# Optimization experiments

Measured on AMD Instinct MI355X. Metric: run time of the kernel, lower is better.

## Reference

```python
import jax, jax.numpy as jnp
import numpy as np

B, S, D, H = 16, 512, 1024, 4096
TOP_K = H // 4  # default: hidden_dim // 4


def setup_inputs() -> dict:
    key = jax.random.key(0)
    ks = jax.random.split(key, 11)
    s = lambda fan_in: 1.0 / np.sqrt(fan_in)
    return {
        "inputs": jax.random.normal(ks[0], (B, S, D), jnp.float32),
        "up_w": jax.random.uniform(ks[1], (H, D), jnp.float32, -s(D), s(D)),
        "up_b": jax.random.uniform(ks[2], (H,), jnp.float32, -s(D), s(D)),
        "gate_w1": jax.random.uniform(ks[3], (H, D), jnp.float32, -s(D), s(D)),
        "gate_b1": jax.random.uniform(ks[4], (H,), jnp.float32, -s(D), s(D)),
        "gate_w2": jax.random.uniform(ks[5], (H, H), jnp.float32, -s(H), s(H)),
        "gate_b2": jax.random.uniform(ks[6], (H,), jnp.float32, -s(H), s(H)),
        "mod_w": jax.random.uniform(ks[7], (H, D), jnp.float32, -s(D), s(D)),
        "mod_b": jax.random.uniform(ks[8], (H,), jnp.float32, -s(D), s(D)),
        "down_w": jax.random.uniform(ks[9], (D, H), jnp.float32, -s(H), s(H)),
        "down_b": jax.random.uniform(ks[10], (D,), jnp.float32, -s(H), s(H)),
    }


def reference(inputs, up_w, up_b, gate_w1, gate_b1, gate_w2, gate_b2,
              mod_w, mod_b, down_w, down_b):
    b, s_len, d = inputs.shape
    h_dim = up_w.shape[0]
    # gate MLP -> scores [B, S, H]
    scores = jax.nn.relu(jnp.einsum('bsd,hd->bsh', inputs, gate_w1) + gate_b1)
    scores = jnp.einsum('bsh,gh->bsg', scores, gate_w2) + gate_b2
    flat = scores.reshape(b, s_len * h_dim)
    k = min(TOP_K * s_len, s_len * h_dim)
    _, flat_idx = jax.lax.top_k(flat, k)                    # [B, k]
    hidden_idx = flat_idx % h_dim                           # [B, k]
    # mask[b, h] = True if row h of up.weight was overwritten by mod.weight
    # (duplicate indices write the same value, so set-semantics are exact)
    mask = jnp.zeros((b, h_dim), bool).at[
        jnp.arange(b)[:, None], hidden_idx].set(True)       # [B, H]
    # Instead of materializing per-batch [B,H,D] weights, compute both shared-
    # weight GEMMs and select per (batch, hidden) row — identical math.
    h_up = jnp.einsum('bsd,hd->bsh', inputs, up_w) + up_b
    h_mod = jnp.einsum('bsd,hd->bsh', inputs, mod_w) + mod_b
    h = jnp.where(mask[:, None, :], h_mod, h_up)            # [B, S, H]
    h = jax.nn.silu(h)
    # dropout is identity in eval/reference mode
    return jnp.einsum('bsh,dh->bsd', h, down_w) + down_b
```

## Files before the change

kernel.cpp:

```cpp
#include <hip/hip_runtime.h>
#include <cstdint>

typedef __attribute__((ext_vector_type(4))) _Float16 f16x4;
typedef __attribute__((ext_vector_type(8))) _Float16 f16x8;
typedef __attribute__((ext_vector_type(4))) float f32x4;

#define D_DIM 1024
#define H_DIM 4096
#define BS_ROWS 8192
#define K_SEL 524288u
#define CAND_CAP 32768u

__device__ __forceinline__ unsigned lkey(float v){
  float u = fmaf(v, 67108864.f, 268435456.f);
  u = fminf(fmaxf(u, 0.f), 536870911.f);
  return (unsigned)u;
}

__device__ __forceinline__ void gload16(const _Float16* g, _Float16* l){
  __builtin_amdgcn_global_load_lds(
      (const __attribute__((address_space(1))) void*)g,
      (__attribute__((address_space(3))) void*)l, 16, 0, 0);
}

template<int N> __device__ __forceinline__ void waitcnt_vm(){
  if      constexpr (N == 0) asm volatile("s_waitcnt vmcnt(0)" ::: "memory");
  else if constexpr (N == 4) asm volatile("s_waitcnt vmcnt(4)" ::: "memory");
  else if constexpr (N == 6) asm volatile("s_waitcnt vmcnt(6)" ::: "memory");
  else                       asm volatile("s_waitcnt vmcnt(8)" ::: "memory");
}

__device__ __forceinline__ size_t img_g32(int row, int k8, int nkt32){
  int p = (row & 127) >> 1;
  int s = (((row & 1) << 2) | (k8 & 3)) ^ (p & 7);
  return ((size_t)((row >> 7) * nkt32 + (k8 >> 2)) << 9) + (p << 3) + s;
}

__global__ __launch_bounds__(256)
void pack_all(const float* __restrict__ X, const float* __restrict__ g1w,
              const float* __restrict__ g2w, const float* __restrict__ upw,
              const float* __restrict__ modw, const float* __restrict__ dww,
              _Float16* __restrict__ Xhi, _Float16* __restrict__ Xlo,
              _Float16* __restrict__ G1hi, _Float16* __restrict__ G1lo,
              _Float16* __restrict__ G2hi, _Float16* __restrict__ G2lo,
              _Float16* __restrict__ UPhi, _Float16* __restrict__ MODhi,
              _Float16* __restrict__ DWhi)
{
  unsigned g = blockIdx.x * 256u + threadIdx.x;
  const float* W; _Float16* hi; _Float16* lo = nullptr;
  int k8s, n32; unsigned base;
  if      (g < 1048576u){ W=X;    hi=Xhi;  lo=Xlo;  k8s=7; n32=32;  base=0u;        }
  else if (g < 1572864u){ W=g1w;  hi=G1hi; lo=G1lo; k8s=7; n32=32;  base=1048576u; }
  else if (g < 3670016u){ W=g2w;  hi=G2hi; lo=G2lo; k8s=9; n32=128; base=1572864u; }
  else if (g < 4194304u){ W=upw;  hi=UPhi;          k8s=7; n32=32;  base=3670016u; }
  else if (g < 4718592u){ W=modw; hi=MODhi;         k8s=7; n32=32;  base=4194304u; }
  else                  { W=dww;  hi=DWhi;          k8s=9; n32=128; base=4718592u; }
  g -= base;
  int row = (int)(g >> k8s), k8 = (int)(g & ((1u << k8s) - 1u));
  const float* src = W + ((size_t)row << (k8s + 3)) + (k8 << 3);
  float4 f0 = *(const float4*)src, f1 = *(const float4*)(src + 4);
  float ff[8] = {f0.x,f0.y,f0.z,f0.w,f1.x,f1.y,f1.z,f1.w};
  f16x8 hv, lv;
  #pragma unroll
  for (int i = 0; i < 8; i++){
    hv[i] = (_Float16)ff[i];
    lv[i] = (_Float16)(ff[i] - (float)hv[i]);
  }
  size_t d = img_g32(row, k8, n32) << 3;
  *(f16x8*)&hi[d] = hv;
  if (lo) *(f16x8*)&lo[d] = lv;
}

enum { MODE_G1 = 0, MODE_G2 = 1, MODE_UPMOD = 2, MODE_DOWN = 3 };

template<int MODE>
__global__ __launch_bounds__(256)
void gemm_t(const _Float16* __restrict__ Ahi, const _Float16* __restrict__ Alo,
            const _Float16* __restrict__ Bhi, const _Float16* __restrict__ Blo,
            const float* __restrict__ bias0, const float* __restrict__ bias1,
            const unsigned* __restrict__ mask,
            _Float16* __restrict__ Chi, _Float16* __restrict__ Clo,
            float* __restrict__ C32,
            unsigned* __restrict__ keys, unsigned* __restrict__ Mkey,
            unsigned* __restrict__ hist,
            int N, int K, int m_img_base, int c_row_base, int batch_base)
{
  constexpr int NSEG = (MODE == MODE_G1) ? 3 : 1;
  constexpr bool BSEL = (MODE == MODE_UPMOD);
  constexpr int NLD = (NSEG == 3) ? 8 : (BSEL ? 6 : 4);
  __shared__ __align__(16) _Float16 sA [2][4096];
  __shared__ __align__(16) _Float16 sB [2][4096];
  __shared__ __align__(16) _Float16 sAl[NSEG >= 2 ? 2 : 1][NSEG >= 2 ? 4096 : 8];
  __shared__ __align__(16) _Float16 sBl[(NSEG == 3 || BSEL) ? 2 : 1][(NSEG == 3 || BSEL) ? 4096 : 8];
  __shared__ unsigned lh[MODE == MODE_G2 ? 4096 : 1];

  const int nbx = gridDim.x;
  int wg = blockIdx.y * nbx + blockIdx.x;
  const int nwg = nbx * gridDim.y;
  wg = (wg & 7) * (nwg >> 3) + (wg >> 3);
  const int bx = wg % nbx, by = wg / nbx;

  const int tid = threadIdx.x;
  const int lane = tid & 63;
  const int w  = tid >> 6;
  const int wr = w >> 1, wc = w & 1;
  const int lr = lane & 15;
  const int q  = lane >> 4;

  const int m0 = m_img_base + by * 128;
  const int n0 = bx * 128;
  const int nkt = K >> 5;
  const size_t arow = (size_t)(m0 >> 7) * nkt;
  const size_t brow = (size_t)(n0 >> 7) * nkt;

  const _Float16* bbase[4];
  if (BSEL){
    const int bb = m0 >> 9;
    #pragma unroll
    for (int i = 0; i < 4; i++){
      int row = wc*64 + i*16 + lr;
      bbase[i] = mask[bb * H_DIM + n0 + row] ? &sBl[0][0] : &sB[0][0];
    }
    waitcnt_vm<0>();
  }

  f32x4 acc[4][4];
  #pragma unroll
  for (int i = 0; i < 4; i++)
    #pragma unroll
    for (int j = 0; j < 4; j++) acc[i][j] = (f32x4){0.f,0.f,0.f,0.f};

  const int soff = (((((lr & 1) << 2) | q) ^ (lr >> 1)) << 3);

  auto STAGE = [&](int buf, int kt){
    const _Float16* at = Ahi + ((arow + kt) << 12);
    #pragma unroll
    for (int j = 0; j < 2; j++)
      gload16(at + ((w*2 + j) << 9) + (lane << 3), &sA[buf][(w*2 + j) << 9]);
    if (NSEG >= 2){
      const _Float16* alt = Alo + ((arow + kt) << 12);
      const _Float16* bht = Bhi + ((brow + kt) << 12);
      #pragma unroll
      for (int j = 0; j < 2; j++){
        gload16(alt + ((w*2 + j) << 9) + (lane << 3), &sAl[buf][(w*2 + j) << 9]);
        gload16(bht + ((w*2 + j) << 9) + (lane << 3), &sB [buf][(w*2 + j) << 9]);
      }
      if (NSEG == 3){
        const _Float16* blt = Blo + ((brow + kt) << 12);
        #pragma unroll
        for (int j = 0; j < 2; j++)
          gload16(blt + ((w*2 + j) << 9) + (lane << 3), &sBl[buf][(w*2 + j) << 9]);
      }
    } else if (BSEL){
      const _Float16* bht = Bhi + ((brow + kt) << 12);
      const _Float16* blt = Blo + ((brow + kt) << 12);
      #pragma unroll
      for (int j = 0; j < 2; j++){
        gload16(bht + ((w*2 + j) << 9) + (lane << 3), &sB [buf][(w*2 + j) << 9]);
        gload16(blt + ((w*2 + j) << 9) + (lane << 3), &sBl[buf][(w*2 + j) << 9]);
      }
    } else {
      const _Float16* bht = Bhi + ((brow + kt) << 12);
      #pragma unroll
      for (int j = 0; j < 2; j++)
        gload16(bht + ((w*2 + j) << 9) + (lane << 3), &sB[buf][(w*2 + j) << 9]);
    }
  };

  STAGE(0, 0);
  int cur = 0;
  for (int kt = 0; kt < nkt; ++kt){
    if (kt + 1 < nkt){ STAGE(cur ^ 1, kt + 1); waitcnt_vm<NLD>(); }
    else             { waitcnt_vm<0>(); }
    __builtin_amdgcn_s_barrier();
    __builtin_amdgcn_sched_barrier(0);

    f16x8 fah[4], fbh[4], fal[4], fbl[4];
    #pragma unroll
    for (int i = 0; i < 4; i++){
      const int ap = ((wr*32 + i*8 + (lr >> 1)) << 6) + soff;
      const int bp = ((wc*32 + i*8 + (lr >> 1)) << 6) + soff;
      fah[i] = *(const f16x8*)&sA[cur][ap];
      if (BSEL) fbh[i] = *(const f16x8*)(bbase[i] + (cur << 12) + bp);
      else      fbh[i] = *(const f16x8*)&sB[cur][bp];
      if (NSEG >= 2) fal[i] = *(const f16x8*)&sAl[cur][ap];
      if (NSEG == 3) fbl[i] = *(const f16x8*)&sBl[cur][bp];
    }
    #pragma unroll
    for (int mi = 0; mi < 4; mi++)
      #pragma unroll
      for (int ni = 0; ni < 4; ni++)
        acc[mi][ni] = __builtin_amdgcn_mfma_f32_16x16x32_f16(fah[mi], fbh[ni], acc[mi][ni], 0,0,0);
    if (NSEG >= 2){
      #pragma unroll
      for (int mi = 0; mi < 4; mi++)
        #pragma unroll
        for (int ni = 0; ni < 4; ni++)
          acc[mi][ni] = __builtin_amdgcn_mfma_f32_16x16x32_f16(fal[mi], fbh[ni], acc[mi][ni], 0,0,0);
    }
    if (NSEG == 3){
      #pragma unroll
      for (int mi = 0; mi < 4; mi++)
        #pragma unroll
        for (int ni = 0; ni < 4; ni++)
          acc[mi][ni] = __builtin_amdgcn_mfma_f32_16x16x32_f16(fah[mi], fbl[ni], acc[mi][ni], 0,0,0);
    }
    __builtin_amdgcn_s_barrier();
    cur ^= 1;
  }

  if (MODE == MODE_G2){
    __syncthreads();
    for (int i = tid; i < 4096; i += 256) lh[i] = 0;
    __syncthreads();
  }

  #pragma unroll
  for (int ni = 0; ni < 4; ni++){
    const int gc = n0 + wc*64 + ni*16 + lr;
    float bias;
    if (MODE == MODE_UPMOD) bias = mask[(m0 >> 9) * H_DIM + gc] ? bias1[gc] : bias0[gc];
    else                    bias = bias0[gc];
    unsigned colmax = 0u;
    #pragma unroll
    for (int mi = 0; mi < 4; mi++){
      #pragma unroll
      for (int r = 0; r < 4; r++){
        const int gr = m0 + wr*64 + mi*16 + q*4 + r;
        const int cr = gr - c_row_base;
        float v = acc[mi][ni][r] + bias;
        if (MODE == MODE_G1){
          v = fmaxf(v, 0.f);
          _Float16 hh = (_Float16)v;
          size_t d = (img_g32(cr, gc >> 3, N >> 5) << 3) + (gc & 7);
          Chi[d] = hh;
          if (Clo) Clo[d] = (_Float16)(v - (float)hh);
        }
        if (MODE == MODE_UPMOD){
          v = v / (1.f + __expf(-v));
          size_t d = (img_g32(cr, gc >> 3, N >> 5) << 3) + (gc & 7);
          Chi[d] = (_Float16)v;
        }
        if (MODE == MODE_DOWN) C32[(size_t)cr * N + gc] = v;
        if (MODE == MODE_G2){
          unsigned key = lkey(v);
          keys[(size_t)cr * N + gc] = key;
          colmax = max(colmax, key);
          atomicAdd(&lh[key >> 17], 1u);
        }
      }
    }
    if (MODE == MODE_G2)
      atomicMax(&Mkey[(batch_base + (m0 >> 9)) * H_DIM + gc], colmax);
  }

  if (MODE == MODE_G2){
    __syncthreads();
    const int gb = batch_base + (m0 >> 9);
    for (int i = tid; i < 4096; i += 256)
      if (lh[i]) atomicAdd(&hist[(gb << 12) + i], lh[i]);
  }
}


__global__ __launch_bounds__(256)
void select12(const unsigned* __restrict__ hist, unsigned* __restrict__ b12,
              unsigned* __restrict__ krem, unsigned* __restrict__ ccount, int b0)
{
  const int b = b0 + (int)blockIdx.x;
  __shared__ unsigned part[256];
  const unsigned base = (unsigned)b << 12;
  unsigned s = 0;
  #pragma unroll
  for (int i = 0; i < 16; i++) s += hist[base + threadIdx.x*16 + i];
  part[threadIdx.x] = s;
  __syncthreads();
  if (threadIdx.x == 0){
    unsigned cum = 0; int t = 255;
    for (; t > 0; --t){
      if (cum + part[t] >= K_SEL) break;
      cum += part[t];
    }
    int bin = 15; unsigned kr = K_SEL;
    for (; bin > 0; --bin){
      unsigned c = hist[base + t*16 + bin];
      if (cum + c >= K_SEL) break;
      cum += c;
    }
    kr = K_SEL - cum;
    b12[b] = (unsigned)(t*16 + bin);
    krem[b] = kr;
    ccount[b] = 0;
  }
}

__global__ __launch_bounds__(256)
void collect(const unsigned* __restrict__ keys, const unsigned* __restrict__ b12,
             unsigned* __restrict__ cand, unsigned* __restrict__ ccount, int b0)
{
  __shared__ unsigned cbuf[1024];
  __shared__ unsigned lcnt, gbase;
  const int bl = blockIdx.y;
  const int b  = b0 + bl;
  const unsigned bin = b12[b];
  if (threadIdx.x == 0) lcnt = 0;
  __syncthreads();
  const uint4* p = (const uint4*)(keys + (size_t)bl*2097152u + (size_t)blockIdx.x*8192u);
  uint4 kv[8];
  #pragma unroll
  for (int j = 0; j < 8; j++) kv[j] = p[threadIdx.x + j*256];
  #pragma unroll
  for (int j = 0; j < 8; j++){
    #pragma unroll
    for (int e = 0; e < 4; e++){
      unsigned k = (e==0)?kv[j].x:(e==1)?kv[j].y:(e==2)?kv[j].z:kv[j].w;
      if ((k >> 17) == bin){
        unsigned idx = atomicAdd(&lcnt, 1u);
        if (idx < 1024u) cbuf[idx] = k;
      }
    }
  }
  __syncthreads();
  const unsigned n = lcnt < 1024u ? lcnt : 1024u;
  if (threadIdx.x == 0) gbase = atomicAdd(&ccount[b], n);
  __syncthreads();
  const unsigned gb = gbase;
  for (unsigned i = threadIdx.x; i < n; i += 256){
    unsigned dst = gb + i;
    if (dst < CAND_CAP) cand[((size_t)b << 15) + dst] = cbuf[i];
  }
}

__global__ __launch_bounds__(256)
void select_exact(const unsigned* __restrict__ cand, const unsigned* __restrict__ ccount,
                  const unsigned* __restrict__ b12, const unsigned* __restrict__ kremA,
                  unsigned* __restrict__ tkey, int b0)
{
  const int b = b0 + (int)blockIdx.x;
  unsigned cc = ccount[b];
  const unsigned n = cc < CAND_CAP ? cc : CAND_CAP;
  __shared__ unsigned h[256];
  __shared__ unsigned sh2[2];
  unsigned prefix = b12[b] << 17;
  unsigned krem = kremA[b];
  const unsigned pm[3]  = {0xFFFE0000u, 0xFFFFFE00u, 0xFFFFFFFEu};
  const int      shs[3] = {9, 1, 0};
  const int      wid[3] = {256, 256, 2};
  for (int pass = 0; pass < 3; ++pass){
    if (threadIdx.x < (unsigned)wid[pass]) h[threadIdx.x] = 0;
    __syncthreads();
    for (unsigned i = threadIdx.x; i < n; i += 256){
      unsigned k = cand[((size_t)b << 15) + i];
      if ((k & pm[pass]) == prefix)
        atomicAdd(&h[(k >> shs[pass]) & (unsigned)(wid[pass]-1)], 1u);
    }
    __syncthreads();
    if (threadIdx.x == 0){
      unsigned cum = 0; int bin = wid[pass]-1;
      for (; bin > 0; --bin){
        unsigned c = h[bin];
        if (cum + c >= krem) break;
        cum += c;
      }
      krem -= cum;
      prefix |= ((unsigned)bin) << shs[pass];
      sh2[0] = prefix; sh2[1] = krem;
    }
    __syncthreads();
    prefix = sh2[0]; krem = sh2[1];
    __syncthreads();
  }
  if (threadIdx.x == 0) tkey[b] = prefix;
}

__global__ __launch_bounds__(256)
void make_mask(const unsigned* __restrict__ Mkey, const unsigned* __restrict__ tkey,
               unsigned* __restrict__ mask){
  const int i = blockIdx.x * 256 + threadIdx.x;
  const int b = i >> 12;
  mask[i] = (Mkey[i] >= tkey[b]) ? 1u : 0u;
}

extern "C" void kernel_launch(void* const* d_in, const int* in_sizes, int n_in,
                              void* d_out, int out_size, void* d_ws, size_t ws_size,
                              hipStream_t stream)
{
  (void)in_sizes; (void)n_in; (void)out_size; (void)ws_size;
  const float* X      = (const float*)d_in[0];
  const float* up_w   = (const float*)d_in[1];
  const float* up_b   = (const float*)d_in[2];
  const float* g1w    = (const float*)d_in[3];
  const float* g1b    = (const float*)d_in[4];
  const float* g2w    = (const float*)d_in[5];
  const float* g2b    = (const float*)d_in[6];
  const float* mod_w  = (const float*)d_in[7];
  const float* mod_b  = (const float*)d_in[8];
  const float* down_w = (const float*)d_in[9];
  const float* down_b = (const float*)d_in[10];
  float* out = (float*)d_out;

  char* ws = (char*)d_ws;
  _Float16* Xhi  = (_Float16*)(ws);
  _Float16* Xlo  = (_Float16*)(ws + (16ull<<20));
  _Float16* G1hi = (_Float16*)(ws + (32ull<<20));
  _Float16* G1lo = (_Float16*)(ws + (40ull<<20));
  _Float16* G2hi = (_Float16*)(ws + (48ull<<20));
  _Float16* UPhi = (_Float16*)(ws + (112ull<<20));
  _Float16* MODhi= (_Float16*)(ws + (120ull<<20));
  _Float16* DWhi = (_Float16*)(ws + (128ull<<20));
  _Float16* Fhi  = (_Float16*)(ws + (136ull<<20));
  _Float16* Hbuf = (_Float16*)(ws + (136ull<<20));
  unsigned* keys = (unsigned*)(ws + (200ull<<20));
  char* aux = ws + (232ull<<20);
  unsigned* Mkey  = (unsigned*)(aux);
  unsigned* maskb = (unsigned*)(aux + 262144);
  unsigned* hist  = (unsigned*)(aux + 524288);
  unsigned* cand  = (unsigned*)(aux + 786432);
  unsigned* b12   = (unsigned*)(aux + 786432 + 2097152);
  unsigned* krem  = (unsigned*)(aux + 786432 + 2097152 + 64);
  unsigned* ccnt  = (unsigned*)(aux + 786432 + 2097152 + 128);
  unsigned* tkey  = (unsigned*)(aux + 786432 + 2097152 + 192);

  pack_all<<<20480, 256, 0, stream>>>(X, g1w, g2w, up_w, mod_w, down_w,
                                      Xhi, Xlo, G1hi, G1lo, G2hi, nullptr,
                                      UPhi, MODhi, DWhi);

  hipMemsetAsync(Mkey, 0, 262144, stream);
  hipMemsetAsync(hist, 0, 262144, stream);

  for (int half = 0; half < 2; ++half){
    gemm_t<MODE_G1><<<dim3(32, 32), 256, 0, stream>>>(
        Xhi, Xlo, G1hi, G1lo, g1b, nullptr, nullptr,
        Fhi, nullptr, nullptr, nullptr, nullptr, nullptr,
        H_DIM, D_DIM, half*4096, half*4096, 0);
    for (int qd = 0; qd < 2; ++qd){
      const int b0 = half*8 + qd*4;
      gemm_t<MODE_G2><<<dim3(32, 16), 256, 0, stream>>>(
          Fhi, nullptr, G2hi, nullptr, g2b, nullptr, nullptr,
          nullptr, nullptr, nullptr, keys, Mkey, hist,
          H_DIM, H_DIM, qd*2048, qd*2048, half*8);
      select12<<<4, 256, 0, stream>>>(hist, b12, krem, ccnt, b0);
      collect<<<dim3(256,4), 256, 0, stream>>>(keys, b12, cand, ccnt, b0);
      select_exact<<<4, 256, 0, stream>>>(cand, ccnt, b12, krem, tkey, b0);
    }
  }
  make_mask<<<256, 256, 0, stream>>>(Mkey, tkey, maskb);

  gemm_t<MODE_UPMOD><<<dim3(32, 64), 256, 0, stream>>>(
      Xhi, nullptr, UPhi, MODhi, up_b, mod_b, maskb,
      Hbuf, nullptr, nullptr, nullptr, nullptr, nullptr,
      H_DIM, D_DIM, 0, 0, 0);
  gemm_t<MODE_DOWN><<<dim3(8, 64), 256, 0, stream>>>(
      Hbuf, nullptr, DWhi, nullptr, down_b, nullptr, nullptr,
      nullptr, nullptr, out, nullptr, nullptr, nullptr,
      D_DIM, H_DIM, 0, 0, 0);
}
```

Measured before the change: 1.082 ms.

## Gather selected up/mod weight rows directly into LDS and merge G2 quarter passes

In the up/mod GEMM, each lane now picks the mod or up weight source per row using the mask and loads only that row into one LDS buffer. This replaces staging both weight tiles and selecting at read time, halving B-tile global traffic and LDS use. The G2 GEMM and the top-k selection kernels now run once per half covering 8 batches instead of twice over 4, which means fewer launches and more blocks per launch. The dead low-part store in G1 is removed, and the keys buffer is moved to fit the larger 8-batch layout, which could overlap other workspace regions if sizes are off.

```diff
diff --git a/kernel.cpp b/kernel.cpp
--- a/kernel.cpp
+++ b/kernel.cpp
@@ -87,11 +87,11 @@
 {
   constexpr int NSEG = (MODE == MODE_G1) ? 3 : 1;
   constexpr bool BSEL = (MODE == MODE_UPMOD);
-  constexpr int NLD = (NSEG == 3) ? 8 : (BSEL ? 6 : 4);
+  constexpr int NLD = (NSEG == 3) ? 8 : 4;
   __shared__ __align__(16) _Float16 sA [2][4096];
   __shared__ __align__(16) _Float16 sB [2][4096];
-  __shared__ __align__(16) _Float16 sAl[NSEG >= 2 ? 2 : 1][NSEG >= 2 ? 4096 : 8];
-  __shared__ __align__(16) _Float16 sBl[(NSEG == 3 || BSEL) ? 2 : 1][(NSEG == 3 || BSEL) ? 4096 : 8];
+  __shared__ __align__(16) _Float16 sAl[NSEG == 3 ? 2 : 1][NSEG == 3 ? 4096 : 8];
+  __shared__ __align__(16) _Float16 sBl[NSEG == 3 ? 2 : 1][NSEG == 3 ? 4096 : 8];
   __shared__ unsigned lh[MODE == MODE_G2 ? 4096 : 1];
 
   const int nbx = gridDim.x;
@@ -113,13 +113,15 @@
   const size_t arow = (size_t)(m0 >> 7) * nkt;
   const size_t brow = (size_t)(n0 >> 7) * nkt;
 
-  const _Float16* bbase[4];
+  const _Float16* bsrcl[2];
   if (BSEL){
     const int bb = m0 >> 9;
     #pragma unroll
-    for (int i = 0; i < 4; i++){
-      int row = wc*64 + i*16 + lr;
-      bbase[i] = mask[bb * H_DIM + n0 + row] ? &sBl[0][0] : &sB[0][0];
+    for (int j = 0; j < 2; j++){
+      int gi = (w*2 + j)*64 + lane;
+      int p = gi >> 3, x = (gi & 7) ^ (p & 7);
+      int row = (p << 1) | (x >> 2);
+      bsrcl[j] = (mask[bb * H_DIM + n0 + row] ? Blo : Bhi) + (gi << 3);
     }
     waitcnt_vm<0>();
   }
@@ -137,28 +139,21 @@
     #pragma unroll
     for (int j = 0; j < 2; j++)
       gload16(at + ((w*2 + j) << 9) + (lane << 3), &sA[buf][(w*2 + j) << 9]);
-    if (NSEG >= 2){
+    if (NSEG == 3){
       const _Float16* alt = Alo + ((arow + kt) << 12);
       const _Float16* bht = Bhi + ((brow + kt) << 12);
+      const _Float16* blt = Blo + ((brow + kt) << 12);
       #pragma unroll
       for (int j = 0; j < 2; j++){
         gload16(alt + ((w*2 + j) << 9) + (lane << 3), &sAl[buf][(w*2 + j) << 9]);
         gload16(bht + ((w*2 + j) << 9) + (lane << 3), &sB [buf][(w*2 + j) << 9]);
-      }
-      if (NSEG == 3){
-        const _Float16* blt = Blo + ((brow + kt) << 12);
-        #pragma unroll
-        for (int j = 0; j < 2; j++)
-          gload16(blt + ((w*2 + j) << 9) + (lane << 3), &sBl[buf][(w*2 + j) << 9]);
+        gload16(blt + ((w*2 + j) << 9) + (lane << 3), &sBl[buf][(w*2 + j) << 9]);
       }
     } else if (BSEL){
-      const _Float16* bht = Bhi + ((brow + kt) << 12);
-      const _Float16* blt = Blo + ((brow + kt) << 12);
-      #pragma unroll
-      for (int j = 0; j < 2; j++){
-        gload16(bht + ((w*2 + j) << 9) + (lane << 3), &sB [buf][(w*2 + j) << 9]);
-        gload16(blt + ((w*2 + j) << 9) + (lane << 3), &sBl[buf][(w*2 + j) << 9]);
-      }
+      const size_t toff = (brow + kt) << 12;
+      #pragma unroll
+      for (int j = 0; j < 2; j++)
+        gload16(bsrcl[j] + toff, &sB[buf][(w*2 + j) << 9]);
     } else {
       const _Float16* bht = Bhi + ((brow + kt) << 12);
       #pragma unroll
@@ -181,24 +176,23 @@
       const int ap = ((wr*32 + i*8 + (lr >> 1)) << 6) + soff;
       const int bp = ((wc*32 + i*8 + (lr >> 1)) << 6) + soff;
       fah[i] = *(const f16x8*)&sA[cur][ap];
-      if (BSEL) fbh[i] = *(const f16x8*)(bbase[i] + (cur << 12) + bp);
-      else      fbh[i] = *(const f16x8*)&sB[cur][bp];
-      if (NSEG >= 2) fal[i] = *(const f16x8*)&sAl[cur][ap];
-      if (NSEG == 3) fbl[i] = *(const f16x8*)&sBl[cur][bp];
+      fbh[i] = *(const f16x8*)&sB[cur][bp];
+      if (NSEG == 3){
+        fal[i] = *(const f16x8*)&sAl[cur][ap];
+        fbl[i] = *(const f16x8*)&sBl[cur][bp];
+      }
     }
     #pragma unroll
     for (int mi = 0; mi < 4; mi++)
       #pragma unroll
       for (int ni = 0; ni < 4; ni++)
         acc[mi][ni] = __builtin_amdgcn_mfma_f32_16x16x32_f16(fah[mi], fbh[ni], acc[mi][ni], 0,0,0);
-    if (NSEG >= 2){
+    if (NSEG == 3){
       #pragma unroll
       for (int mi = 0; mi < 4; mi++)
         #pragma unroll
         for (int ni = 0; ni < 4; ni++)
           acc[mi][ni] = __builtin_amdgcn_mfma_f32_16x16x32_f16(fal[mi], fbh[ni], acc[mi][ni], 0,0,0);
-    }
-    if (NSEG == 3){
       #pragma unroll
       for (int mi = 0; mi < 4; mi++)
         #pragma unroll
@@ -231,10 +225,8 @@
         float v = acc[mi][ni][r] + bias;
         if (MODE == MODE_G1){
           v = fmaxf(v, 0.f);
-          _Float16 hh = (_Float16)v;
           size_t d = (img_g32(cr, gc >> 3, N >> 5) << 3) + (gc & 7);
-          Chi[d] = hh;
-          if (Clo) Clo[d] = (_Float16)(v - (float)hh);
+          Chi[d] = (_Float16)v;
         }
         if (MODE == MODE_UPMOD){
           v = v / (1.f + __expf(-v));
@@ -409,8 +401,8 @@
   _Float16* MODhi= (_Float16*)(ws + (120ull<<20));
   _Float16* DWhi = (_Float16*)(ws + (128ull<<20));
   _Float16* Fhi  = (_Float16*)(ws + (136ull<<20));
+  unsigned* keys = (unsigned*)(ws + (168ull<<20));
   _Float16* Hbuf = (_Float16*)(ws + (136ull<<20));
-  unsigned* keys = (unsigned*)(ws + (200ull<<20));
   char* aux = ws + (232ull<<20);
   unsigned* Mkey  = (unsigned*)(aux);
   unsigned* maskb = (unsigned*)(aux + 262144);
@@ -429,20 +421,18 @@
   hipMemsetAsync(hist, 0, 262144, stream);
 
   for (int half = 0; half < 2; ++half){
+    const int b0 = half * 8;
     gemm_t<MODE_G1><<<dim3(32, 32), 256, 0, stream>>>(
         Xhi, Xlo, G1hi, G1lo, g1b, nullptr, nullptr,
         Fhi, nullptr, nullptr, nullptr, nullptr, nullptr,
         H_DIM, D_DIM, half*4096, half*4096, 0);
-    for (int qd = 0; qd < 2; ++qd){
-      const int b0 = half*8 + qd*4;
-      gemm_t<MODE_G2><<<dim3(32, 16), 256, 0, stream>>>(
-          Fhi, nullptr, G2hi, nullptr, g2b, nullptr, nullptr,
-          nullptr, nullptr, nullptr, keys, Mkey, hist,
-          H_DIM, H_DIM, qd*2048, qd*2048, half*8);
-      select12<<<4, 256, 0, stream>>>(hist, b12, krem, ccnt, b0);
-      collect<<<dim3(256,4), 256, 0, stream>>>(keys, b12, cand, ccnt, b0);
-      select_exact<<<4, 256, 0, stream>>>(cand, ccnt, b12, krem, tkey, b0);
-    }
+    gemm_t<MODE_G2><<<dim3(32, 32), 256, 0, stream>>>(
+        Fhi, nullptr, G2hi, nullptr, g2b, nullptr, nullptr,
+        nullptr, nullptr, nullptr, keys, Mkey, hist,
+        H_DIM, H_DIM, 0, 0, b0);
+    select12<<<8, 256, 0, stream>>>(hist, b12, krem, ccnt, b0);
+    collect<<<dim3(256, 8), 256, 0, stream>>>(keys, b12, cand, ccnt, b0);
+    select_exact<<<8, 256, 0, stream>>>(cand, ccnt, b12, krem, tkey, b0);
   }
   make_mask<<<256, 256, 0, stream>>>(Mkey, tkey, maskb);
 
```

Measured after the change: 996.0 us. 1.09x faster.
